# Performance work log

Hardware: AMD Instinct MI355X
Metric: run time of the kernel (lower is better)

## Reference

```python
import jax, jax.numpy as jnp
import numpy as np
import math

D_MODEL, N_HEADS, D_HEAD, D_MLP = 768, 12, 64, 3072
EPS = 1e-5
IGNORE = -100000.0


def _ln(x, w, b):
    mu = jnp.mean(x, axis=-1, keepdims=True)
    xc = x - mu
    scale = jnp.sqrt(jnp.mean(xc * xc, axis=-1, keepdims=True) + EPS)
    return (xc / scale) * w + b


def _gelu_new(x):
    # GPT-2 'new' gelu
    return 0.5 * x * (1.0 + jnp.tanh(jnp.sqrt(2.0 / jnp.pi) * (x + 0.044715 * x ** 3)))


def setup_inputs() -> dict:
    key = jax.random.key(0)
    ks = jax.random.split(key, 12)
    std = 0.02
    inp = {
        "resid_pre": jax.random.normal(ks[0], (8, 1024, D_MODEL), jnp.float32),
        "W_Q": jax.random.normal(ks[1], (N_HEADS, D_MODEL, D_HEAD), jnp.float32) * std,
        "b_Q": jnp.zeros((N_HEADS, D_HEAD), jnp.float32),
        "W_K": jax.random.normal(ks[2], (N_HEADS, D_MODEL, D_HEAD), jnp.float32) * std,
        "b_K": jnp.zeros((N_HEADS, D_HEAD), jnp.float32),
        "W_V": jax.random.normal(ks[3], (N_HEADS, D_MODEL, D_HEAD), jnp.float32) * std,
        "b_V": jnp.zeros((N_HEADS, D_HEAD), jnp.float32),
        "W_O": jax.random.normal(ks[4], (N_HEADS, D_HEAD, D_MODEL), jnp.float32) * std,
        "b_O": jnp.zeros((D_MODEL,), jnp.float32),
        "ln1_w": jnp.ones((D_MODEL,), jnp.float32),
        "ln1_b": jnp.zeros((D_MODEL,), jnp.float32),
        "ln2_w": jnp.ones((D_MODEL,), jnp.float32),
        "ln2_b": jnp.zeros((D_MODEL,), jnp.float32),
        "W_in": jax.random.normal(ks[5], (D_MODEL, D_MLP), jnp.float32) * std,
        "b_in": jnp.zeros((D_MLP,), jnp.float32),
        "W_out": jax.random.normal(ks[6], (D_MLP, D_MODEL), jnp.float32) * std,
        "b_out": jnp.zeros((D_MODEL,), jnp.float32),
    }
    return inp


def reference(resid_pre, W_Q, b_Q, W_K, b_K, W_V, b_V, W_O, b_O,
              ln1_w, ln1_b, ln2_w, ln2_b, W_in, b_in, W_out, b_out):
    # ---- ln1 + attention ----
    n = _ln(resid_pre, ln1_w, ln1_b)  # [b, s, d]; broadcast over heads in einsums
    q = jnp.einsum('bsd,hde->bshe', n, W_Q) + b_Q
    k = jnp.einsum('bsd,hde->bshe', n, W_K) + b_K
    v = jnp.einsum('bsd,hde->bshe', n, W_V) + b_V
    scores = jnp.einsum('bqhe,bkhe->bhqk', q, k) / math.sqrt(D_HEAD)
    S = scores.shape[-1]
    causal = jnp.triu(jnp.ones((S, S), dtype=bool), k=1)
    scores = jnp.where(causal, IGNORE, scores)
    pattern = jax.nn.softmax(scores, axis=-1)
    z = jnp.einsum('bhqk,bkhe->bqhe', pattern, v)
    # per-head output with b_O / n_heads each (as in source), then summed over heads
    attn_per_head = jnp.einsum('bqhe,hed->bqhd', z, W_O) + b_O / N_HEADS
    attn_out = attn_per_head.sum(axis=2)  # [b, s, d]
    resid_mid = resid_pre + attn_out
    # ---- ln2 + mlp ----
    n2 = _ln(resid_mid, ln2_w, ln2_b)
    pre = jnp.einsum('bsd,dm->bsm', n2, W_in) + b_in
    post = _gelu_new(pre)
    mlp_out = jnp.einsum('bsm,md->bsd', post, W_out) + b_out
    return resid_mid + mlp_out
```

## Files before the change

### kernel.cpp

```cpp
#include <hip/hip_runtime.h>
#include <hip/hip_bf16.h>

typedef unsigned short u16;
typedef float f32x4 __attribute__((ext_vector_type(4)));
typedef __bf16 bf16x8 __attribute__((ext_vector_type(8)));
typedef unsigned short u16x8 __attribute__((ext_vector_type(8)));
typedef unsigned short u16x4 __attribute__((ext_vector_type(4)));

__device__ __forceinline__ float b2f(u16 u) {
    unsigned v = ((unsigned)u) << 16;
    return __builtin_bit_cast(float, v);
}
__device__ __forceinline__ u16 f2b(float f) {
    unsigned u = __builtin_bit_cast(unsigned, f);
    u += 0x7fffu + ((u >> 16) & 1u);
    return (u16)(u >> 16);
}
__device__ __forceinline__ bf16x8 ldfrag(const u16* p) {
    return __builtin_bit_cast(bf16x8, *(const u16x8*)p);
}
__device__ __forceinline__ f32x4 mfma16(bf16x8 a, bf16x8 b, f32x4 c) {
    return __builtin_amdgcn_mfma_f32_16x16x32_bf16(a, b, c, 0, 0, 0);
}
__device__ __forceinline__ void gload_lds16(const u16* g, u16* l) {
    __builtin_amdgcn_global_load_lds(
        (const __attribute__((address_space(1))) unsigned int*)(g),
        (__attribute__((address_space(3))) unsigned int*)(l), 16, 0, 0);
}

#define T_TOK 8192
#define DM 768
#define NH 12
#define DH 64
#define DMLP 3072
#define SEQ 1024
#define QKV_LD 2304
#define QK_LD 1536

#define OFF_WQKV ((size_t)0)
#define OFF_WO   (OFF_WQKV + (size_t)2304*768)
#define OFF_WIN  (OFF_WO   + (size_t)768*768)
#define OFF_WOUT (OFF_WIN  + (size_t)768*3072)
#define OFF_BQKV (OFF_WOUT + (size_t)3072*768)
#define P0       (OFF_BQKV + (size_t)4608)

#define SZ_N    ((size_t)T_TOK*DM)
#define SZ_QKV  ((size_t)T_TOK*QKV_LD)
#define A_NBUF   (P0)
#define A_QKV    (P0 + SZ_N)
#define A_Z      (P0 + SZ_N + SZ_QKV)
#define A_N2     (P0)
#define A_POST   (P0 + SZ_N)
#define PATHA_BYTES (((size_t)(P0 + SZ_N + SZ_QKV + SZ_N)) * 2)
#define B_Z      (P0)
#define B_QKVB   (P0 + SZ_N)
#define B_NBUF   (B_QKVB + (size_t)SEQ*QKV_LD)
#define B_N2     (P0)
#define B_POSTC  (P0 + SZ_N)

#define PR0 (2304*768)
#define PR1 (768*768)
#define PR2 (768*3072)
#define PR3 (3072*768)
#define PREP_TOTAL (PR0+PR1+PR2+PR3+2304)

__global__ __launch_bounds__(256) void prep_kernel(
    const float* __restrict__ WQ, const float* __restrict__ WK, const float* __restrict__ WV,
    const float* __restrict__ WO, const float* __restrict__ Win, const float* __restrict__ Wout,
    const float* __restrict__ bQ, const float* __restrict__ bK, const float* __restrict__ bV,
    u16* __restrict__ Wqkv_t, u16* __restrict__ Wo_t, u16* __restrict__ Win_t,
    u16* __restrict__ Wout_t, float* __restrict__ bias_qkv)
{
    int idx = blockIdx.x * 256 + threadIdx.x;
    if (idx < PR0) {
        int r = idx / 768, d = idx % 768;
        int which = r / 768;
        int he = r % 768;
        int h = he >> 6, e = he & 63;
        const float* W = (which == 0) ? WQ : ((which == 1) ? WK : WV);
        Wqkv_t[idx] = f2b(W[h * 49152 + d * 64 + e]);
    } else if (idx < PR0 + PR1) {
        int o = idx - PR0;
        int d = o / 768, he = o % 768;
        Wo_t[o] = f2b(WO[he * 768 + d]);
    } else if (idx < PR0 + PR1 + PR2) {
        int o = idx - PR0 - PR1;
        int m = o / 768, d = o % 768;
        Win_t[o] = f2b(Win[d * 3072 + m]);
    } else if (idx < PR0 + PR1 + PR2 + PR3) {
        int o = idx - PR0 - PR1 - PR2;
        int d = o / 3072, m = o % 3072;
        Wout_t[o] = f2b(Wout[m * 768 + d]);
    } else if (idx < PREP_TOTAL) {
        int j = idx - (PR0 + PR1 + PR2 + PR3);
        bias_qkv[j] = (j < 768) ? bQ[j] : ((j < 1536) ? bK[j - 768] : bV[j - 1536]);
    }
}

__global__ __launch_bounds__(256) void ln_kernel(
    const float* __restrict__ x, const float* __restrict__ w,
    const float* __restrict__ bb, u16* __restrict__ out)
{
    __shared__ float red[4];
    size_t base = (size_t)blockIdx.x * DM;
    int tid = threadIdx.x;
    float v0 = x[base + tid], v1 = x[base + tid + 256], v2 = x[base + tid + 512];
    float s = v0 + v1 + v2;
#pragma unroll
    for (int off = 32; off > 0; off >>= 1) s += __shfl_xor(s, off);
    if ((tid & 63) == 0) red[tid >> 6] = s;
    __syncthreads();
    float mu = (red[0] + red[1] + red[2] + red[3]) * (1.0f / 768.0f);
    v0 -= mu; v1 -= mu; v2 -= mu;
    float q = v0 * v0 + v1 * v1 + v2 * v2;
    __syncthreads();
#pragma unroll
    for (int off = 32; off > 0; off >>= 1) q += __shfl_xor(q, off);
    if ((tid & 63) == 0) red[tid >> 6] = q;
    __syncthreads();
    float var = (red[0] + red[1] + red[2] + red[3]) * (1.0f / 768.0f);
    float sc = rsqrtf(var + 1e-5f);
    out[base + tid]       = f2b(v0 * sc * w[tid]       + bb[tid]);
    out[base + tid + 256] = f2b(v1 * sc * w[tid + 256] + bb[tid + 256]);
    out[base + tid + 512] = f2b(v2 * sc * w[tid + 512] + bb[tid + 512]);
}

template <int EPI, int TM>
__global__ __launch_bounds__(256) void gemm_bt_kernel(
    const u16* __restrict__ A, const u16* __restrict__ BT,
    const float* __restrict__ bias, const float* __restrict__ aux,
    void* __restrict__ outp, int N, int K)
{
    __shared__ __align__(16) u16 As[3][TM * 32];
    __shared__ __align__(16) u16 Bs[3][128 * 32];
    const int tid = threadIdx.x;
    const int w = tid >> 6, l = tid & 63;
    const int lr = l & 15, lq = l >> 4;
    const int bm = blockIdx.x * TM, bn = blockIdx.y * 128;
    constexpr int MT = TM / 32;
    constexpr bool TR = (EPI != 4);
    const int wm = (w >> 1) * (TM / 2), wn = (w & 1) * 64;

    f32x4 acc[MT][4];
#pragma unroll
    for (int i = 0; i < MT; i++)
#pragma unroll
        for (int j = 0; j < 4; j++) acc[i][j] = f32x4{0.f, 0.f, 0.f, 0.f};

    const int srow_a = (TM == 128) ? (w * 32 + (l >> 2)) : (w * 16 + (l >> 2));
    const int srow_b = w * 32 + (l >> 2);
    const int scol = (l & 3) * 8;
    const u16* Ab = A  + (size_t)(bm + srow_a) * K + scol;
    const u16* Bb = BT + (size_t)(bn + srow_b) * K + scol;
    const int asd = (TM == 128) ? w * 1024 : w * 512;
    const int bsd = w * 1024;

    const int kiter = K >> 5;

#define STAGE_T(kk, s)                                                      \
    {   const int k0_ = (kk) * 32;                                          \
        gload_lds16(Ab + k0_, &As[s][asd]);                                 \
        if (TM == 128) gload_lds16(Ab + 16 * K + k0_, &As[s][asd + 512]);   \
        gload_lds16(Bb + k0_,          &Bs[s][bsd]);                        \
        gload_lds16(Bb + 16 * K + k0_, &Bs[s][bsd + 512]);  }

    STAGE_T(0, 0);
    STAGE_T(1, 1);

    int cur = 0;
    for (int t = 0; t < kiter; ++t) {
        if (t + 1 < kiter) {
            if constexpr (TM == 128) asm volatile("s_waitcnt vmcnt(4)" ::: "memory");
            else                     asm volatile("s_waitcnt vmcnt(3)" ::: "memory");
        } else {
            asm volatile("s_waitcnt vmcnt(0)" ::: "memory");
        }
        __builtin_amdgcn_s_barrier();
        __builtin_amdgcn_sched_barrier(0);

        const u16* Asc = &As[cur][0];
        const u16* Bsc = &Bs[cur][0];
        bf16x8 af[MT], bf[4];
#pragma unroll
        for (int mt = 0; mt < MT; mt++) af[mt] = ldfrag(&Asc[(wm + mt * 16 + lr) * 32 + lq * 8]);
#pragma unroll
        for (int nt = 0; nt < 4; nt++) bf[nt] = ldfrag(&Bsc[(wn + nt * 16 + lr) * 32 + lq * 8]);
#pragma unroll
        for (int mt = 0; mt < MT; mt++)
#pragma unroll
            for (int nt = 0; nt < 4; nt++)
                acc[mt][nt] = TR ? mfma16(bf[nt], af[mt], acc[mt][nt])
                                 : mfma16(af[mt], bf[nt], acc[mt][nt]);

        if (t + 2 < kiter) {
            int nb = cur + 2; if (nb >= 3) nb -= 3;
            STAGE_T(t + 2, nb);
        }
        cur = (cur + 1 == 3) ? 0 : cur + 1;
    }
#undef STAGE_T

    if (EPI == 4) {
        const bool isv = (bn >= 1536);
        u16* vtg = (u16*)aux;
#pragma unroll
        for (int mt = 0; mt < MT; mt++) {
            int row0 = bm + wm + mt * 16 + lq * 4;
            if (!isv) {
#pragma unroll
                for (int r = 0; r < 4; r++) {
                    size_t ro = (size_t)(row0 + r) * QK_LD;
#pragma unroll
                    for (int nt = 0; nt < 4; nt++) {
                        int col = bn + wn + nt * 16 + lr;
                        ((u16*)outp)[ro + col] = f2b(acc[mt][nt][r] + bias[col]);
                    }
                }
            } else {
                int bloc = row0 >> 10;
                int s = row0 & 1023;
#pragma unroll
                for (int nt = 0; nt < 4; nt++) {
                    int col = bn + wn + nt * 16 + lr;
                    int he = col - 1536;
                    float bcol = bias[col];
                    u16x4 pk;
                    pk[0] = f2b(acc[mt][nt][0] + bcol);
                    pk[1] = f2b(acc[mt][nt][1] + bcol);
                    pk[2] = f2b(acc[mt][nt][2] + bcol);
                    pk[3] = f2b(acc[mt][nt][3] + bcol);
                    *(u16x4*)&vtg[(size_t)bloc * (NH * 64 * SEQ)
                                  + (size_t)he * SEQ + s] = pk;
                }
            }
        }
        return;
    }

#pragma unroll
    for (int mt = 0; mt < MT; mt++) {
        int row = bm + wm + mt * 16 + lr;
        size_t ro = (size_t)row * N;
#pragma unroll
        for (int nt = 0; nt < 4; nt++) {
            int col0 = bn + wn + nt * 16 + lq * 4;
            f32x4 v = acc[mt][nt] + *(const f32x4*)&bias[col0];
            if (EPI == 0) {
                u16x4 pk;
#pragma unroll
                for (int r = 0; r < 4; r++) pk[r] = f2b(v[r]);
                *(u16x4*)&((u16*)outp)[ro + col0] = pk;
            } else if (EPI == 2) {
                u16x4 pk;
#pragma unroll
                for (int r = 0; r < 4; r++) {
                    float x = v[r];
                    float y = 0.7978845608028654f * (x + 0.044715f * x * x * x);
                    pk[r] = f2b(x / (1.0f + __expf(-2.0f * y)));
                }
                *(u16x4*)&((u16*)outp)[ro + col0] = pk;
            } else {
                f32x4 a4 = *(const f32x4*)&aux[ro + col0];
                v += a4;
                *(f32x4*)&((float*)outp)[ro + col0] = v;
            }
        }
    }
}

__global__ __launch_bounds__(256, 5) void attn_kernel(
    const u16* __restrict__ qk, const u16* __restrict__ vtg,
    u16* __restrict__ z, int b0, int bq0)
{
    __shared__ __align__(16) u16 Ks[64 * 72];
    __shared__ __align__(16) u16 Vt[64 * 72];
    __shared__ __align__(16) u16 Ps[4][16 * 72];

    const int qt = (int)(gridDim.x - 1) - (int)blockIdx.x;
    const int bh = blockIdx.y;
    const int b = b0 + bh / NH, h = bh % NH;
    const int tid = threadIdx.x, w = tid >> 6, l = tid & 63;
    const int lr = l & 15, lq = l >> 4;
    const int qbase = qt * 64;
    const u16* qp = qk + (size_t)(b - bq0) * SEQ * QK_LD + h * 64;
    const u16* kp = qp + 768;
    const u16* vthead = vtg + ((size_t)(b - bq0) * NH + h) * (64 * SEQ);
    u16* PsW = &Ps[w][0];

    bf16x8 aq0, aq1;
    {
        const u16* qrow = qp + (size_t)(qbase + w * 16 + lr) * QK_LD + lq * 8;
        aq0 = ldfrag(qrow);
        aq1 = ldfrag(qrow + 32);
    }

    float m_i = -1e30f;
    float l_i = 0.f;
    f32x4 O[4];
#pragma unroll
    for (int i = 0; i < 4; i++) O[i] = f32x4{0.f, 0.f, 0.f, 0.f};

    const int nkt = qt + 1;
    const int srow = tid >> 2;
    const int spart = (tid & 3) * 16;

    u16x8 kreg0, kreg1, vreg0, vreg1;
    {
        const u16* ks = kp + (size_t)srow * QK_LD + spart;
        kreg0 = *(const u16x8*)ks;
        kreg1 = *(const u16x8*)(ks + 8);
        const u16* vs = vthead + (size_t)srow * SEQ + spart;
        vreg0 = *(const u16x8*)vs;
        vreg1 = *(const u16x8*)(vs + 8);
    }

    for (int kt = 0; kt < nkt; ++kt) {
        __syncthreads();
        *(u16x8*)&Ks[srow * 72 + spart]     = kreg0;
        *(u16x8*)&Ks[srow * 72 + spart + 8] = kreg1;
        *(u16x8*)&Vt[srow * 72 + spart]     = vreg0;
        *(u16x8*)&Vt[srow * 72 + spart + 8] = vreg1;
        __syncthreads();
        if (kt + 1 < nkt) {
            const u16* ks = kp + (size_t)((kt + 1) * 64 + srow) * QK_LD + spart;
            kreg0 = *(const u16x8*)ks;
            kreg1 = *(const u16x8*)(ks + 8);
            const u16* vs = vthead + (size_t)srow * SEQ + (kt + 1) * 64 + spart;
            vreg0 = *(const u16x8*)vs;
            vreg1 = *(const u16x8*)(vs + 8);
        }

        f32x4 S[4];
#pragma unroll
        for (int nt = 0; nt < 4; nt++) S[nt] = f32x4{0.f, 0.f, 0.f, 0.f};
#pragma unroll
        for (int nt = 0; nt < 4; nt++) {
            bf16x8 bk0 = ldfrag(&Ks[(nt * 16 + lr) * 72 + lq * 8]);
            bf16x8 bk1 = ldfrag(&Ks[(nt * 16 + lr) * 72 + 32 + lq * 8]);
            S[nt] = mfma16(bk0, aq0, S[nt]);
            S[nt] = mfma16(bk1, aq1, S[nt]);
        }

        const bool diag = (kt == qt);
        float mx = -1e30f;
#pragma unroll
        for (int nt = 0; nt < 4; nt++)
#pragma unroll
            for (int r = 0; r < 4; r++) {
                float sv = S[nt][r] * 0.125f;
                if (diag) sv = (nt * 16 + lq * 4 + r <= w * 16 + lr) ? sv : -1e30f;
                S[nt][r] = sv;
                mx = fmaxf(mx, sv);
            }
        mx = fmaxf(mx, __shfl_xor(mx, 16));
        mx = fmaxf(mx, __shfl_xor(mx, 32));
        float mn = fmaxf(m_i, mx);
        float alpha = __expf(m_i - mn);
        m_i = mn;
        float rs = 0.f;
#pragma unroll
        for (int nt = 0; nt < 4; nt++) {
            u16x4 pk;
#pragma unroll
            for (int r = 0; r < 4; r++) {
                float pe = __expf(S[nt][r] - mn);
                rs += pe;
                pk[r] = f2b(pe);
            }
            *(u16x4*)&PsW[lr * 72 + nt * 16 + lq * 4] = pk;
        }
        rs += __shfl_xor(rs, 16);
        rs += __shfl_xor(rs, 32);
        l_i = l_i * alpha + rs;

#pragma unroll
        for (int r = 0; r < 4; r++) {
            float ar = __shfl(alpha, (l & 48) | (lq * 4 + r));
            O[0][r] *= ar; O[1][r] *= ar; O[2][r] *= ar; O[3][r] *= ar;
        }

#pragma unroll
        for (int kq = 0; kq < 2; kq++) {
            bf16x8 ap = ldfrag(&PsW[lr * 72 + kq * 32 + lq * 8]);
#pragma unroll
            for (int ot = 0; ot < 4; ot++) {
                bf16x8 bv = ldfrag(&Vt[(ot * 16 + lr) * 72 + kq * 32 + lq * 8]);
                O[ot] = mfma16(ap, bv, O[ot]);
            }
        }
    }

    float li[4];
#pragma unroll
    for (int r = 0; r < 4; r++)
        li[r] = __shfl(l_i, (l & 48) | (lq * 4 + r));
#pragma unroll
    for (int ot = 0; ot < 4; ot++)
#pragma unroll
        for (int r = 0; r < 4; r++) {
            int q = qbase + w * 16 + lq * 4 + r;
            size_t t = (size_t)b * SEQ + q;
            z[t * DM + h * 64 + ot * 16 + lr] = f2b(O[ot][r] / li[r]);
        }
}

extern "C" void kernel_launch(void* const* d_in, const int* in_sizes, int n_in,
                              void* d_out, int out_size, void* d_ws, size_t ws_size,
                              hipStream_t stream) {
    const float* resid_pre = (const float*)d_in[0];
    const float* W_Q  = (const float*)d_in[1];
    const float* b_Q  = (const float*)d_in[2];
    const float* W_K  = (const float*)d_in[3];
    const float* b_K  = (const float*)d_in[4];
    const float* W_V  = (const float*)d_in[5];
    const float* b_V  = (const float*)d_in[6];
    const float* W_O  = (const float*)d_in[7];
    const float* b_O  = (const float*)d_in[8];
    const float* ln1w = (const float*)d_in[9];
    const float* ln1b = (const float*)d_in[10];
    const float* ln2w = (const float*)d_in[11];
    const float* ln2b = (const float*)d_in[12];
    const float* W_in  = (const float*)d_in[13];
    const float* b_in  = (const float*)d_in[14];
    const float* W_out = (const float*)d_in[15];
    const float* b_out = (const float*)d_in[16];

    u16* ws16       = (u16*)d_ws;
    u16* Wqkv_t     = ws16 + OFF_WQKV;
    u16* Wo_t       = ws16 + OFF_WO;
    u16* Win_t      = ws16 + OFF_WIN;
    u16* Wout_t     = ws16 + OFF_WOUT;
    float* bias_qkv = (float*)(ws16 + OFF_BQKV);
    float* outp  = (float*)d_out;
    float* resid = (float*)d_out;

    prep_kernel<<<(PREP_TOTAL + 255) / 256, 256, 0, stream>>>(
        W_Q, W_K, W_V, W_O, W_in, W_out, b_Q, b_K, b_V,
        Wqkv_t, Wo_t, Win_t, Wout_t, bias_qkv);

    if (ws_size >= PATHA_BYTES) {
        u16* nbuf    = ws16 + A_NBUF;
        u16* qkbuf   = ws16 + A_QKV;
        u16* vtgA    = ws16 + A_QKV + (size_t)T_TOK * QK_LD;
        u16* zbuf    = ws16 + A_Z;
        u16* n2buf   = ws16 + A_N2;
        u16* postbuf = ws16 + A_POST;

        ln_kernel<<<T_TOK, 256, 0, stream>>>(resid_pre, ln1w, ln1b, nbuf);
        gemm_bt_kernel<4, 128><<<dim3(T_TOK / 128, QKV_LD / 128), 256, 0, stream>>>(
            nbuf, Wqkv_t, bias_qkv, (const float*)vtgA, qkbuf, QKV_LD, DM);
        attn_kernel<<<dim3(SEQ / 64, 8 * NH), 256, 0, stream>>>(qkbuf, vtgA, zbuf, 0, 0);
        gemm_bt_kernel<1, 64><<<dim3(T_TOK / 64, DM / 128), 256, 0, stream>>>(
            zbuf, Wo_t, b_O, resid_pre, resid, DM, DM);
        ln_kernel<<<T_TOK, 256, 0, stream>>>(resid, ln2w, ln2b, n2buf);
        gemm_bt_kernel<2, 128><<<dim3(T_TOK / 128, DMLP / 128), 256, 0, stream>>>(
            n2buf, Win_t, b_in, nullptr, postbuf, DMLP, DM);
        gemm_bt_kernel<3, 64><<<dim3(T_TOK / 64, DM / 128), 256, 0, stream>>>(
            postbuf, Wout_t, b_out, resid, outp, DM, DMLP);
    } else {
        u16* zbuf   = ws16 + B_Z;
        u16* qkb    = ws16 + B_QKVB;
        u16* vtgB   = qkb + (size_t)SEQ * QK_LD;
        u16* nbuf   = ws16 + B_NBUF;
        u16* n2buf  = ws16 + B_N2;
        u16* postc  = ws16 + B_POSTC;

        ln_kernel<<<T_TOK, 256, 0, stream>>>(resid_pre, ln1w, ln1b, nbuf);
        for (int b = 0; b < 8; b++) {
            gemm_bt_kernel<4, 128><<<dim3(SEQ / 128, QKV_LD / 128), 256, 0, stream>>>(
                nbuf + (size_t)b * SEQ * DM, Wqkv_t, bias_qkv, (const float*)vtgB, qkb, QKV_LD, DM);
            attn_kernel<<<dim3(SEQ / 64, NH), 256, 0, stream>>>(qkb, vtgB, zbuf, b, b);
        }
        gemm_bt_kernel<1, 64><<<dim3(T_TOK / 64, DM / 128), 256, 0, stream>>>(
            zbuf, Wo_t, b_O, resid_pre, resid, DM, DM);
        ln_kernel<<<T_TOK, 256, 0, stream>>>(resid, ln2w, ln2b, n2buf);
        for (int c = 0; c < 4; c++) {
            const size_t r0 = (size_t)c * 2048;
            gemm_bt_kernel<2, 128><<<dim3(2048 / 128, DMLP / 128), 256, 0, stream>>>(
                n2buf + r0 * DM, Win_t, b_in, nullptr, postc, DMLP, DM);
            gemm_bt_kernel<3, 64><<<dim3(2048 / 64, DM / 128), 256, 0, stream>>>(
                postc, Wout_t, b_out, resid + r0 * DM, outp + r0 * DM, DM, DMLP);
        }
    }
}
```

Measured before the change: 423.7 us.

## Make GEMM kernel loop over output tiles with fixed grid and MFMA priority

The GEMM kernel now takes M and walks tiles in a grid-stride loop, so each block may compute several output tiles. The QKV and MLP-in launches use half as many blocks as tiles, and the other launches keep one tile per block. It also raises wave priority around the MFMA block with s_setprio. The aim is to cut block launch and scheduling overhead and keep the matrix units fed, at the cost of losing latency hiding from extra resident blocks and carrying serialized tiles per block.

```diff
diff --git a/kernel.cpp b/kernel.cpp
--- a/kernel.cpp
+++ b/kernel.cpp
@@ -129,143 +129,151 @@
 __global__ __launch_bounds__(256) void gemm_bt_kernel(
     const u16* __restrict__ A, const u16* __restrict__ BT,
     const float* __restrict__ bias, const float* __restrict__ aux,
-    void* __restrict__ outp, int N, int K)
+    void* __restrict__ outp, int M, int N, int K)
 {
-    __shared__ __align__(16) u16 As[3][TM * 32];
-    __shared__ __align__(16) u16 Bs[3][128 * 32];
+    constexpr int DEPTH = 3;
+    __shared__ __align__(16) u16 As[DEPTH][TM * 32];
+    __shared__ __align__(16) u16 Bs[DEPTH][128 * 32];
     const int tid = threadIdx.x;
     const int w = tid >> 6, l = tid & 63;
     const int lr = l & 15, lq = l >> 4;
-    const int bm = blockIdx.x * TM, bn = blockIdx.y * 128;
     constexpr int MT = TM / 32;
     constexpr bool TR = (EPI != 4);
     const int wm = (w >> 1) * (TM / 2), wn = (w & 1) * 64;
 
-    f32x4 acc[MT][4];
-#pragma unroll
-    for (int i = 0; i < MT; i++)
-#pragma unroll
-        for (int j = 0; j < 4; j++) acc[i][j] = f32x4{0.f, 0.f, 0.f, 0.f};
-
     const int srow_a = (TM == 128) ? (w * 32 + (l >> 2)) : (w * 16 + (l >> 2));
     const int srow_b = w * 32 + (l >> 2);
     const int scol = (l & 3) * 8;
-    const u16* Ab = A  + (size_t)(bm + srow_a) * K + scol;
-    const u16* Bb = BT + (size_t)(bn + srow_b) * K + scol;
     const int asd = (TM == 128) ? w * 1024 : w * 512;
     const int bsd = w * 1024;
 
+    const int mTiles = M / TM;
+    const int tiles = mTiles * (N >> 7);
     const int kiter = K >> 5;
 
 #define STAGE_T(kk, s)                                                      \
     {   const int k0_ = (kk) * 32;                                          \
         gload_lds16(Ab + k0_, &As[s][asd]);                                 \
-        if (TM == 128) gload_lds16(Ab + 16 * K + k0_, &As[s][asd + 512]);   \
+        if constexpr (TM == 128) gload_lds16(Ab + 16 * K + k0_, &As[s][asd + 512]); \
         gload_lds16(Bb + k0_,          &Bs[s][bsd]);                        \
         gload_lds16(Bb + 16 * K + k0_, &Bs[s][bsd + 512]);  }
 
-    STAGE_T(0, 0);
-    STAGE_T(1, 1);
-
-    int cur = 0;
-    for (int t = 0; t < kiter; ++t) {
-        if (t + 1 < kiter) {
-            if constexpr (TM == 128) asm volatile("s_waitcnt vmcnt(4)" ::: "memory");
-            else                     asm volatile("s_waitcnt vmcnt(3)" ::: "memory");
-        } else {
-            asm volatile("s_waitcnt vmcnt(0)" ::: "memory");
-        }
-        __builtin_amdgcn_s_barrier();
-        __builtin_amdgcn_sched_barrier(0);
-
-        const u16* Asc = &As[cur][0];
-        const u16* Bsc = &Bs[cur][0];
-        bf16x8 af[MT], bf[4];
-#pragma unroll
-        for (int mt = 0; mt < MT; mt++) af[mt] = ldfrag(&Asc[(wm + mt * 16 + lr) * 32 + lq * 8]);
-#pragma unroll
-        for (int nt = 0; nt < 4; nt++) bf[nt] = ldfrag(&Bsc[(wn + nt * 16 + lr) * 32 + lq * 8]);
-#pragma unroll
-        for (int mt = 0; mt < MT; mt++)
-#pragma unroll
-            for (int nt = 0; nt < 4; nt++)
-                acc[mt][nt] = TR ? mfma16(bf[nt], af[mt], acc[mt][nt])
-                                 : mfma16(af[mt], bf[nt], acc[mt][nt]);
-
-        if (t + 2 < kiter) {
-            int nb = cur + 2; if (nb >= 3) nb -= 3;
-            STAGE_T(t + 2, nb);
-        }
-        cur = (cur + 1 == 3) ? 0 : cur + 1;
-    }
-#undef STAGE_T
-
-    if (EPI == 4) {
-        const bool isv = (bn >= 1536);
-        u16* vtg = (u16*)aux;
-#pragma unroll
-        for (int mt = 0; mt < MT; mt++) {
-            int row0 = bm + wm + mt * 16 + lq * 4;
-            if (!isv) {
-#pragma unroll
-                for (int r = 0; r < 4; r++) {
-                    size_t ro = (size_t)(row0 + r) * QK_LD;
+    for (int tix = blockIdx.x; tix < tiles; tix += gridDim.x) {
+        const int bm = (tix % mTiles) * TM;
+        const int bn = (tix / mTiles) * 128;
+        const u16* Ab = A  + (size_t)(bm + srow_a) * K + scol;
+        const u16* Bb = BT + (size_t)(bn + srow_b) * K + scol;
+
+        f32x4 acc[MT][4];
+#pragma unroll
+        for (int i = 0; i < MT; i++)
+#pragma unroll
+            for (int j = 0; j < 4; j++) acc[i][j] = f32x4{0.f, 0.f, 0.f, 0.f};
+
+        STAGE_T(0, 0);
+        STAGE_T(1, 1);
+
+        int cur = 0;
+        for (int t = 0; t < kiter; ++t) {
+            if (t + 1 < kiter) {
+                if constexpr (TM == 128) asm volatile("s_waitcnt vmcnt(4)" ::: "memory");
+                else                     asm volatile("s_waitcnt vmcnt(3)" ::: "memory");
+            } else {
+                asm volatile("s_waitcnt vmcnt(0)" ::: "memory");
+            }
+            __builtin_amdgcn_s_barrier();
+            __builtin_amdgcn_sched_barrier(0);
+
+            const u16* Asc = &As[cur][0];
+            const u16* Bsc = &Bs[cur][0];
+            bf16x8 af[MT], bf[4];
+#pragma unroll
+            for (int mt = 0; mt < MT; mt++) af[mt] = ldfrag(&Asc[(wm + mt * 16 + lr) * 32 + lq * 8]);
+#pragma unroll
+            for (int nt = 0; nt < 4; nt++) bf[nt] = ldfrag(&Bsc[(wn + nt * 16 + lr) * 32 + lq * 8]);
+            __builtin_amdgcn_s_setprio(1);
+#pragma unroll
+            for (int mt = 0; mt < MT; mt++)
+#pragma unroll
+                for (int nt = 0; nt < 4; nt++)
+                    acc[mt][nt] = TR ? mfma16(bf[nt], af[mt], acc[mt][nt])
+                                     : mfma16(af[mt], bf[nt], acc[mt][nt]);
+            __builtin_amdgcn_s_setprio(0);
+
+            if (t + 2 < kiter) {
+                int nb = cur + 2; if (nb >= 3) nb -= 3;
+                STAGE_T(t + 2, nb);
+            }
+            cur = (cur + 1 == 3) ? 0 : cur + 1;
+        }
+
+        if (EPI == 4) {
+            const bool isv = (bn >= 1536);
+            u16* vtg = (u16*)aux;
+#pragma unroll
+            for (int mt = 0; mt < MT; mt++) {
+                int row0 = bm + wm + mt * 16 + lq * 4;
+                if (!isv) {
+#pragma unroll
+                    for (int r = 0; r < 4; r++) {
+                        size_t ro = (size_t)(row0 + r) * QK_LD;
+#pragma unroll
+                        for (int nt = 0; nt < 4; nt++) {
+                            int col = bn + wn + nt * 16 + lr;
+                            ((u16*)outp)[ro + col] = f2b(acc[mt][nt][r] + bias[col]);
+                        }
+                    }
+                } else {
+                    int bloc = row0 >> 10;
+                    int s = row0 & 1023;
 #pragma unroll
                     for (int nt = 0; nt < 4; nt++) {
                         int col = bn + wn + nt * 16 + lr;
-                        ((u16*)outp)[ro + col] = f2b(acc[mt][nt][r] + bias[col]);
+                        int he = col - 1536;
+                        float bcol = bias[col];
+                        u16x4 pk;
+                        pk[0] = f2b(acc[mt][nt][0] + bcol);
+                        pk[1] = f2b(acc[mt][nt][1] + bcol);
+                        pk[2] = f2b(acc[mt][nt][2] + bcol);
+                        pk[3] = f2b(acc[mt][nt][3] + bcol);
+                        *(u16x4*)&vtg[(size_t)bloc * (NH * 64 * SEQ)
+                                      + (size_t)he * SEQ + s] = pk;
                     }
                 }
-            } else {
-                int bloc = row0 >> 10;
-                int s = row0 & 1023;
+            }
+        } else {
+#pragma unroll
+            for (int mt = 0; mt < MT; mt++) {
+                int row = bm + wm + mt * 16 + lr;
+                size_t ro = (size_t)row * N;
 #pragma unroll
                 for (int nt = 0; nt < 4; nt++) {
-                    int col = bn + wn + nt * 16 + lr;
-                    int he = col - 1536;
-                    float bcol = bias[col];
-                    u16x4 pk;
-                    pk[0] = f2b(acc[mt][nt][0] + bcol);
-                    pk[1] = f2b(acc[mt][nt][1] + bcol);
-                    pk[2] = f2b(acc[mt][nt][2] + bcol);
-                    pk[3] = f2b(acc[mt][nt][3] + bcol);
-                    *(u16x4*)&vtg[(size_t)bloc * (NH * 64 * SEQ)
-                                  + (size_t)he * SEQ + s] = pk;
+                    int col0 = bn + wn + nt * 16 + lq * 4;
+                    f32x4 v = acc[mt][nt] + *(const f32x4*)&bias[col0];
+                    if (EPI == 0) {
+                        u16x4 pk;
+#pragma unroll
+                        for (int r = 0; r < 4; r++) pk[r] = f2b(v[r]);
+                        *(u16x4*)&((u16*)outp)[ro + col0] = pk;
+                    } else if (EPI == 2) {
+                        u16x4 pk;
+#pragma unroll
+                        for (int r = 0; r < 4; r++) {
+                            float x = v[r];
+                            float y = 0.7978845608028654f * (x + 0.044715f * x * x * x);
+                            pk[r] = f2b(x / (1.0f + __expf(-2.0f * y)));
+                        }
+                        *(u16x4*)&((u16*)outp)[ro + col0] = pk;
+                    } else {
+                        f32x4 a4 = *(const f32x4*)&aux[ro + col0];
+                        v += a4;
+                        *(f32x4*)&((float*)outp)[ro + col0] = v;
+                    }
                 }
             }
         }
-        return;
-    }
-
-#pragma unroll
-    for (int mt = 0; mt < MT; mt++) {
-        int row = bm + wm + mt * 16 + lr;
-        size_t ro = (size_t)row * N;
-#pragma unroll
-        for (int nt = 0; nt < 4; nt++) {
-            int col0 = bn + wn + nt * 16 + lq * 4;
-            f32x4 v = acc[mt][nt] + *(const f32x4*)&bias[col0];
-            if (EPI == 0) {
-                u16x4 pk;
-#pragma unroll
-                for (int r = 0; r < 4; r++) pk[r] = f2b(v[r]);
-                *(u16x4*)&((u16*)outp)[ro + col0] = pk;
-            } else if (EPI == 2) {
-                u16x4 pk;
-#pragma unroll
-                for (int r = 0; r < 4; r++) {
-                    float x = v[r];
-                    float y = 0.7978845608028654f * (x + 0.044715f * x * x * x);
-                    pk[r] = f2b(x / (1.0f + __expf(-2.0f * y)));
-                }
-                *(u16x4*)&((u16*)outp)[ro + col0] = pk;
-            } else {
-                f32x4 a4 = *(const f32x4*)&aux[ro + col0];
-                v += a4;
-                *(f32x4*)&((float*)outp)[ro + col0] = v;
-            }
-        }
-    }
+    }
+#undef STAGE_T
 }
 
 __global__ __launch_bounds__(256, 5) void attn_kernel(
@@ -447,16 +455,16 @@
         u16* postbuf = ws16 + A_POST;
 
         ln_kernel<<<T_TOK, 256, 0, stream>>>(resid_pre, ln1w, ln1b, nbuf);
-        gemm_bt_kernel<4, 128><<<dim3(T_TOK / 128, QKV_LD / 128), 256, 0, stream>>>(
-            nbuf, Wqkv_t, bias_qkv, (const float*)vtgA, qkbuf, QKV_LD, DM);
+        gemm_bt_kernel<4, 128><<<576, 256, 0, stream>>>(
+            nbuf, Wqkv_t, bias_qkv, (const float*)vtgA, qkbuf, T_TOK, QKV_LD, DM);
         attn_kernel<<<dim3(SEQ / 64, 8 * NH), 256, 0, stream>>>(qkbuf, vtgA, zbuf, 0, 0);
-        gemm_bt_kernel<1, 64><<<dim3(T_TOK / 64, DM / 128), 256, 0, stream>>>(
-            zbuf, Wo_t, b_O, resid_pre, resid, DM, DM);
+        gemm_bt_kernel<1, 64><<<768, 256, 0, stream>>>(
+            zbuf, Wo_t, b_O, resid_pre, resid, T_TOK, DM, DM);
         ln_kernel<<<T_TOK, 256, 0, stream>>>(resid, ln2w, ln2b, n2buf);
-        gemm_bt_kernel<2, 128><<<dim3(T_TOK / 128, DMLP / 128), 256, 0, stream>>>(
-            n2buf, Win_t, b_in, nullptr, postbuf, DMLP, DM);
-        gemm_bt_kernel<3, 64><<<dim3(T_TOK / 64, DM / 128), 256, 0, stream>>>(
-            postbuf, Wout_t, b_out, resid, outp, DM, DMLP);
+        gemm_bt_kernel<2, 128><<<768, 256, 0, stream>>>(
+            n2buf, Win_t, b_in, nullptr, postbuf, T_TOK, DMLP, DM);
+        gemm_bt_kernel<3, 64><<<768, 256, 0, stream>>>(
+            postbuf, Wout_t, b_out, resid, outp, T_TOK, DM, DMLP);
     } else {
         u16* zbuf   = ws16 + B_Z;
         u16* qkb    = ws16 + B_QKVB;
@@ -467,19 +475,20 @@
 
         ln_kernel<<<T_TOK, 256, 0, stream>>>(resid_pre, ln1w, ln1b, nbuf);
         for (int b = 0; b < 8; b++) {
-            gemm_bt_kernel<4, 128><<<dim3(SEQ / 128, QKV_LD / 128), 256, 0, stream>>>(
-                nbuf + (size_t)b * SEQ * DM, Wqkv_t, bias_qkv, (const float*)vtgB, qkb, QKV_LD, DM);
+            gemm_bt_kernel<4, 128><<<144, 256, 0, stream>>>(
+                nbuf + (size_t)b * SEQ * DM, Wqkv_t, bias_qkv, (const float*)vtgB,
+                qkb, SEQ, QKV_LD, DM);
             attn_kernel<<<dim3(SEQ / 64, NH), 256, 0, stream>>>(qkb, vtgB, zbuf, b, b);
         }
-        gemm_bt_kernel<1, 64><<<dim3(T_TOK / 64, DM / 128), 256, 0, stream>>>(
-            zbuf, Wo_t, b_O, resid_pre, resid, DM, DM);
+        gemm_bt_kernel<1, 64><<<768, 256, 0, stream>>>(
+            zbuf, Wo_t, b_O, resid_pre, resid, T_TOK, DM, DM);
         ln_kernel<<<T_TOK, 256, 0, stream>>>(resid, ln2w, ln2b, n2buf);
         for (int c = 0; c < 4; c++) {
             const size_t r0 = (size_t)c * 2048;
-            gemm_bt_kernel<2, 128><<<dim3(2048 / 128, DMLP / 128), 256, 0, stream>>>(
-                n2buf + r0 * DM, Win_t, b_in, nullptr, postc, DMLP, DM);
-            gemm_bt_kernel<3, 64><<<dim3(2048 / 64, DM / 128), 256, 0, stream>>>(
-                postc, Wout_t, b_out, resid + r0 * DM, outp + r0 * DM, DM, DMLP);
-        }
-    }
-}
+            gemm_bt_kernel<2, 128><<<384, 256, 0, stream>>>(
+                n2buf + r0 * DM, Win_t, b_in, nullptr, postc, 2048, DMLP, DM);
+            gemm_bt_kernel<3, 64><<<192, 256, 0, stream>>>(
+                postc, Wout_t, b_out, resid + r0 * DM, outp + r0 * DM, 2048, DM, DMLP);
+        }
+    }
+}
```

Result: slower. 443.2 us (+4.6%).

## Tile weight-prep transpose via LDS and double query rows per attention block

Applied to the files above, without the earlier changes.

The weight prep kernel now transposes 64x64 tiles through shared memory, so it reads and writes in coalesced rows instead of doing one strided gather per element. The attention kernel now covers 128 query rows per block, two 16-row groups per wave, so each K/V tile loaded into shared memory serves twice as many queries. Groups that lie fully above the causal diagonal are skipped. The cost is more registers (launch bounds hint lowered from 5 to 4 blocks), half as many attention blocks, and a more uneven causal workload across blocks.

```diff
diff --git a/kernel.cpp b/kernel.cpp
--- a/kernel.cpp
+++ b/kernel.cpp
@@ -58,11 +58,10 @@
 #define B_N2     (P0)
 #define B_POSTC  (P0 + SZ_N)
 
-#define PR0 (2304*768)
-#define PR1 (768*768)
-#define PR2 (768*3072)
-#define PR3 (3072*768)
-#define PREP_TOTAL (PR0+PR1+PR2+PR3+2304)
+#define TT_QKV  432
+#define TT_WO   (TT_QKV + 144)
+#define TT_WIN  (TT_WO + 576)
+#define TT_WOUT (TT_WIN + 576)
 
 __global__ __launch_bounds__(256) void prep_kernel(
     const float* __restrict__ WQ, const float* __restrict__ WK, const float* __restrict__ WV,
@@ -71,29 +70,50 @@
     u16* __restrict__ Wqkv_t, u16* __restrict__ Wo_t, u16* __restrict__ Win_t,
     u16* __restrict__ Wout_t, float* __restrict__ bias_qkv)
 {
-    int idx = blockIdx.x * 256 + threadIdx.x;
-    if (idx < PR0) {
-        int r = idx / 768, d = idx % 768;
-        int which = r / 768;
-        int he = r % 768;
-        int h = he >> 6, e = he & 63;
+    const int bid = blockIdx.x;
+    const int tid = threadIdx.x;
+    if (bid == TT_WOUT) {
+        for (int j = tid; j < 2304; j += 256)
+            bias_qkv[j] = (j < 768) ? bQ[j] : ((j < 1536) ? bK[j - 768] : bV[j - 1536]);
+        return;
+    }
+    __shared__ u16 tile[64][72];
+
+    const float* sp; u16* dp;
+    int sldc, dldc;
+    if (bid < TT_QKV) {
+        int wh = bid / 12, td = bid % 12;
+        int which = wh / 12, h = wh % 12;
         const float* W = (which == 0) ? WQ : ((which == 1) ? WK : WV);
-        Wqkv_t[idx] = f2b(W[h * 49152 + d * 64 + e]);
-    } else if (idx < PR0 + PR1) {
-        int o = idx - PR0;
-        int d = o / 768, he = o % 768;
-        Wo_t[o] = f2b(WO[he * 768 + d]);
-    } else if (idx < PR0 + PR1 + PR2) {
-        int o = idx - PR0 - PR1;
-        int m = o / 768, d = o % 768;
-        Win_t[o] = f2b(Win[d * 3072 + m]);
-    } else if (idx < PR0 + PR1 + PR2 + PR3) {
-        int o = idx - PR0 - PR1 - PR2;
-        int d = o / 3072, m = o % 3072;
-        Wout_t[o] = f2b(Wout[m * 768 + d]);
-    } else if (idx < PREP_TOTAL) {
-        int j = idx - (PR0 + PR1 + PR2 + PR3);
-        bias_qkv[j] = (j < 768) ? bQ[j] : ((j < 1536) ? bK[j - 768] : bV[j - 1536]);
+        sp = W + (size_t)h * 49152 + (size_t)(td * 64) * 64;   sldc = 64;
+        dp = Wqkv_t + (size_t)(which * 768 + h * 64) * 768 + td * 64; dldc = 768;
+    } else if (bid < TT_WO) {
+        int t2 = bid - TT_QKV, ti = t2 / 12, tj = t2 % 12;
+        sp = WO + (size_t)(ti * 64) * 768 + tj * 64;           sldc = 768;
+        dp = Wo_t + (size_t)(tj * 64) * 768 + ti * 64;         dldc = 768;
+    } else if (bid < TT_WIN) {
+        int t3 = bid - TT_WO, ti = t3 / 48, tj = t3 % 48;
+        sp = Win + (size_t)(ti * 64) * 3072 + tj * 64;         sldc = 3072;
+        dp = Win_t + (size_t)(tj * 64) * 768 + ti * 64;        dldc = 768;
+    } else {
+        int t4 = bid - TT_WIN, ti = t4 / 12, tj = t4 % 12;
+        sp = Wout + (size_t)(ti * 64) * 768 + tj * 64;         sldc = 768;
+        dp = Wout_t + (size_t)(tj * 64) * 3072 + ti * 64;      dldc = 3072;
+    }
+
+    {
+        int r = tid >> 2, cseg = (tid & 3) * 16;
+        const float* src = sp + (size_t)r * sldc + cseg;
+#pragma unroll
+        for (int j = 0; j < 16; j++)
+            tile[cseg + j][r] = f2b(src[j]);
+    }
+    __syncthreads();
+    {
+        int r2 = tid >> 2, c2seg = (tid & 3) * 16;
+        u16* dst = dp + (size_t)r2 * dldc + c2seg;
+        *(u16x8*)dst       = *(const u16x8*)&tile[r2][c2seg];
+        *(u16x8*)(dst + 8) = *(const u16x8*)&tile[r2][c2seg + 8];
     }
 }
 
@@ -160,7 +180,7 @@
 #define STAGE_T(kk, s)                                                      \
     {   const int k0_ = (kk) * 32;                                          \
         gload_lds16(Ab + k0_, &As[s][asd]);                                 \
-        if (TM == 128) gload_lds16(Ab + 16 * K + k0_, &As[s][asd + 512]);   \
+        if constexpr (TM == 128) gload_lds16(Ab + 16 * K + k0_, &As[s][asd + 512]); \
         gload_lds16(Bb + k0_,          &Bs[s][bsd]);                        \
         gload_lds16(Bb + 16 * K + k0_, &Bs[s][bsd + 512]);  }
 
@@ -268,7 +288,7 @@
     }
 }
 
-__global__ __launch_bounds__(256, 5) void attn_kernel(
+__global__ __launch_bounds__(256, 4) void attn_kernel(
     const u16* __restrict__ qk, const u16* __restrict__ vtg,
     u16* __restrict__ z, int b0, int bq0)
 {
@@ -281,26 +301,29 @@
     const int b = b0 + bh / NH, h = bh % NH;
     const int tid = threadIdx.x, w = tid >> 6, l = tid & 63;
     const int lr = l & 15, lq = l >> 4;
-    const int qbase = qt * 64;
+    const int qbase = qt * 128;
     const u16* qp = qk + (size_t)(b - bq0) * SEQ * QK_LD + h * 64;
     const u16* kp = qp + 768;
     const u16* vthead = vtg + ((size_t)(b - bq0) * NH + h) * (64 * SEQ);
     u16* PsW = &Ps[w][0];
 
-    bf16x8 aq0, aq1;
-    {
-        const u16* qrow = qp + (size_t)(qbase + w * 16 + lr) * QK_LD + lq * 8;
-        aq0 = ldfrag(qrow);
-        aq1 = ldfrag(qrow + 32);
-    }
-
-    float m_i = -1e30f;
-    float l_i = 0.f;
-    f32x4 O[4];
-#pragma unroll
-    for (int i = 0; i < 4; i++) O[i] = f32x4{0.f, 0.f, 0.f, 0.f};
-
-    const int nkt = qt + 1;
+    bf16x8 aq[2][2];
+#pragma unroll
+    for (int g = 0; g < 2; g++) {
+        const u16* qrow = qp + (size_t)(qbase + w * 32 + g * 16 + lr) * QK_LD + lq * 8;
+        aq[g][0] = ldfrag(qrow);
+        aq[g][1] = ldfrag(qrow + 32);
+    }
+
+    float m_i[2] = {-1e30f, -1e30f};
+    float l_i[2] = {0.f, 0.f};
+    f32x4 O[2][4];
+#pragma unroll
+    for (int g = 0; g < 2; g++)
+#pragma unroll
+        for (int i = 0; i < 4; i++) O[g][i] = f32x4{0.f, 0.f, 0.f, 0.f};
+
+    const int nkt = 2 * qt + 2;
     const int srow = tid >> 2;
     const int spart = (tid & 3) * 16;
 
@@ -330,78 +353,89 @@
             vreg1 = *(const u16x8*)(vs + 8);
         }
 
-        f32x4 S[4];
-#pragma unroll
-        for (int nt = 0; nt < 4; nt++) S[nt] = f32x4{0.f, 0.f, 0.f, 0.f};
-#pragma unroll
-        for (int nt = 0; nt < 4; nt++) {
-            bf16x8 bk0 = ldfrag(&Ks[(nt * 16 + lr) * 72 + lq * 8]);
-            bf16x8 bk1 = ldfrag(&Ks[(nt * 16 + lr) * 72 + 32 + lq * 8]);
-            S[nt] = mfma16(bk0, aq0, S[nt]);
-            S[nt] = mfma16(bk1, aq1, S[nt]);
-        }
-
-        const bool diag = (kt == qt);
-        float mx = -1e30f;
-#pragma unroll
-        for (int nt = 0; nt < 4; nt++)
+        const int krel = kt * 64 - qbase;
+
+#pragma unroll
+        for (int g = 0; g < 2; g++) {
+            const int gq0 = w * 32 + g * 16;
+            if (krel >= gq0 + 16) continue;
+
+            f32x4 S[4];
+#pragma unroll
+            for (int nt = 0; nt < 4; nt++) S[nt] = f32x4{0.f, 0.f, 0.f, 0.f};
+#pragma unroll
+            for (int nt = 0; nt < 4; nt++) {
+                bf16x8 bk0 = ldfrag(&Ks[(nt * 16 + lr) * 72 + lq * 8]);
+                bf16x8 bk1 = ldfrag(&Ks[(nt * 16 + lr) * 72 + 32 + lq * 8]);
+                S[nt] = mfma16(bk0, aq[g][0], S[nt]);
+                S[nt] = mfma16(bk1, aq[g][1], S[nt]);
+            }
+
+            const bool diag = (krel + 63 > gq0);
+            float mx = -1e30f;
+#pragma unroll
+            for (int nt = 0; nt < 4; nt++)
+#pragma unroll
+                for (int r = 0; r < 4; r++) {
+                    float sv = S[nt][r] * 0.125f;
+                    if (diag) sv = (krel + nt * 16 + lq * 4 + r <= gq0 + lr) ? sv : -1e30f;
+                    S[nt][r] = sv;
+                    mx = fmaxf(mx, sv);
+                }
+            mx = fmaxf(mx, __shfl_xor(mx, 16));
+            mx = fmaxf(mx, __shfl_xor(mx, 32));
+            float mn = fmaxf(m_i[g], mx);
+            float alpha = __expf(m_i[g] - mn);
+            m_i[g] = mn;
+            float rs = 0.f;
+#pragma unroll
+            for (int nt = 0; nt < 4; nt++) {
+                u16x4 pk;
+#pragma unroll
+                for (int r = 0; r < 4; r++) {
+                    float pe = __expf(S[nt][r] - mn);
+                    rs += pe;
+                    pk[r] = f2b(pe);
+                }
+                *(u16x4*)&PsW[lr * 72 + nt * 16 + lq * 4] = pk;
+            }
+            rs += __shfl_xor(rs, 16);
+            rs += __shfl_xor(rs, 32);
+            l_i[g] = l_i[g] * alpha + rs;
+
 #pragma unroll
             for (int r = 0; r < 4; r++) {
-                float sv = S[nt][r] * 0.125f;
-                if (diag) sv = (nt * 16 + lq * 4 + r <= w * 16 + lr) ? sv : -1e30f;
-                S[nt][r] = sv;
-                mx = fmaxf(mx, sv);
-            }
-        mx = fmaxf(mx, __shfl_xor(mx, 16));
-        mx = fmaxf(mx, __shfl_xor(mx, 32));
-        float mn = fmaxf(m_i, mx);
-        float alpha = __expf(m_i - mn);
-        m_i = mn;
-        float rs = 0.f;
-#pragma unroll
-        for (int nt = 0; nt < 4; nt++) {
-            u16x4 pk;
+                float ar = __shfl(alpha, (l & 48) | (lq * 4 + r));
+                O[g][0][r] *= ar; O[g][1][r] *= ar; O[g][2][r] *= ar; O[g][3][r] *= ar;
+            }
+
+#pragma unroll
+            for (int kq = 0; kq < 2; kq++) {
+                bf16x8 ap = ldfrag(&PsW[lr * 72 + kq * 32 + lq * 8]);
+#pragma unroll
+                for (int ot = 0; ot < 4; ot++) {
+                    bf16x8 bv = ldfrag(&Vt[(ot * 16 + lr) * 72 + kq * 32 + lq * 8]);
+                    O[g][ot] = mfma16(ap, bv, O[g][ot]);
+                }
+            }
+        }
+    }
+
+#pragma unroll
+    for (int g = 0; g < 2; g++) {
+        float li[4];
+#pragma unroll
+        for (int r = 0; r < 4; r++)
+            li[r] = __shfl(l_i[g], (l & 48) | (lq * 4 + r));
+#pragma unroll
+        for (int ot = 0; ot < 4; ot++)
 #pragma unroll
             for (int r = 0; r < 4; r++) {
-                float pe = __expf(S[nt][r] - mn);
-                rs += pe;
-                pk[r] = f2b(pe);
-            }
-            *(u16x4*)&PsW[lr * 72 + nt * 16 + lq * 4] = pk;
-        }
-        rs += __shfl_xor(rs, 16);
-        rs += __shfl_xor(rs, 32);
-        l_i = l_i * alpha + rs;
-
-#pragma unroll
-        for (int r = 0; r < 4; r++) {
-            float ar = __shfl(alpha, (l & 48) | (lq * 4 + r));
-            O[0][r] *= ar; O[1][r] *= ar; O[2][r] *= ar; O[3][r] *= ar;
-        }
-
-#pragma unroll
-        for (int kq = 0; kq < 2; kq++) {
-            bf16x8 ap = ldfrag(&PsW[lr * 72 + kq * 32 + lq * 8]);
-#pragma unroll
-            for (int ot = 0; ot < 4; ot++) {
-                bf16x8 bv = ldfrag(&Vt[(ot * 16 + lr) * 72 + kq * 32 + lq * 8]);
-                O[ot] = mfma16(ap, bv, O[ot]);
-            }
-        }
-    }
-
-    float li[4];
-#pragma unroll
-    for (int r = 0; r < 4; r++)
-        li[r] = __shfl(l_i, (l & 48) | (lq * 4 + r));
-#pragma unroll
-    for (int ot = 0; ot < 4; ot++)
-#pragma unroll
-        for (int r = 0; r < 4; r++) {
-            int q = qbase + w * 16 + lq * 4 + r;
-            size_t t = (size_t)b * SEQ + q;
-            z[t * DM + h * 64 + ot * 16 + lr] = f2b(O[ot][r] / li[r]);
-        }
+                int q = qbase + w * 32 + g * 16 + lq * 4 + r;
+                size_t t = (size_t)b * SEQ + q;
+                z[t * DM + h * 64 + ot * 16 + lr] = f2b(O[g][ot][r] / li[r]);
+            }
+    }
 }
 
 extern "C" void kernel_launch(void* const* d_in, const int* in_sizes, int n_in,
@@ -434,7 +468,7 @@
     float* outp  = (float*)d_out;
     float* resid = (float*)d_out;
 
-    prep_kernel<<<(PREP_TOTAL + 255) / 256, 256, 0, stream>>>(
+    prep_kernel<<<TT_WOUT + 1, 256, 0, stream>>>(
         W_Q, W_K, W_V, W_O, W_in, W_out, b_Q, b_K, b_V,
         Wqkv_t, Wo_t, Win_t, Wout_t, bias_qkv);
 
@@ -449,7 +483,7 @@
         ln_kernel<<<T_TOK, 256, 0, stream>>>(resid_pre, ln1w, ln1b, nbuf);
         gemm_bt_kernel<4, 128><<<dim3(T_TOK / 128, QKV_LD / 128), 256, 0, stream>>>(
             nbuf, Wqkv_t, bias_qkv, (const float*)vtgA, qkbuf, QKV_LD, DM);
-        attn_kernel<<<dim3(SEQ / 64, 8 * NH), 256, 0, stream>>>(qkbuf, vtgA, zbuf, 0, 0);
+        attn_kernel<<<dim3(SEQ / 128, 8 * NH), 256, 0, stream>>>(qkbuf, vtgA, zbuf, 0, 0);
         gemm_bt_kernel<1, 64><<<dim3(T_TOK / 64, DM / 128), 256, 0, stream>>>(
             zbuf, Wo_t, b_O, resid_pre, resid, DM, DM);
         ln_kernel<<<T_TOK, 256, 0, stream>>>(resid, ln2w, ln2b, n2buf);
@@ -469,7 +503,7 @@
         for (int b = 0; b < 8; b++) {
             gemm_bt_kernel<4, 128><<<dim3(SEQ / 128, QKV_LD / 128), 256, 0, stream>>>(
                 nbuf + (size_t)b * SEQ * DM, Wqkv_t, bias_qkv, (const float*)vtgB, qkb, QKV_LD, DM);
-            attn_kernel<<<dim3(SEQ / 64, NH), 256, 0, stream>>>(qkb, vtgB, zbuf, b, b);
+            attn_kernel<<<dim3(SEQ / 128, NH), 256, 0, stream>>>(qkb, vtgB, zbuf, b, b);
         }
         gemm_bt_kernel<1, 64><<<dim3(T_TOK / 64, DM / 128), 256, 0, stream>>>(
             zbuf, Wo_t, b_O, resid_pre, resid, DM, DM);
```

After: 413.5 us. 2.4% less time.
